# Kernel optimization log

Measured on AMD Instinct MI355X. Metric: run time of the kernel, lower is better.

The kernel has to match this reference:

```python
import jax, jax.numpy as jnp
import numpy as np

B, L, D = 4, 2048, 1024


def setup_inputs() -> dict:
    key = jax.random.key(0)
    ks = jax.random.split(key, 7)
    scale = 1.0 / np.sqrt(D)
    x = jax.random.normal(ks[0], (B, L, D), dtype=jnp.float32)
    wq = jax.random.normal(ks[1], (D, D), dtype=jnp.float32) * scale
    wk = jax.random.normal(ks[2], (D, D), dtype=jnp.float32) * scale
    wv = jax.random.normal(ks[3], (D, D), dtype=jnp.float32) * scale
    bq = jnp.zeros((D,), dtype=jnp.float32)
    bk = jnp.zeros((D,), dtype=jnp.float32)
    bv = jnp.zeros((D,), dtype=jnp.float32)
    # causal decoder mask, shape [B, 1, L, L] as produced by nn.make_causal_mask
    causal = jnp.tril(jnp.ones((L, L), dtype=bool))
    mask = jnp.broadcast_to(causal[None, None, :, :], (B, 1, L, L))
    return {"x": x, "mask": mask, "wq": wq, "bq": bq, "wk": wk, "bk": bk, "wv": wv, "bv": bv}


def reference(x, mask, wq, bq, wk, bk, wv, bv):
    # q/k/v projections (Dense with bias)
    q = x @ wq + bq            # [B, L, D]
    k = x @ wk + bk
    v = x @ wv + bv
    depth = q.shape[-1]
    q = q / jnp.sqrt(jnp.asarray(depth, dtype=q.dtype))
    attn = jnp.einsum('bqd,bkd->bqk', q, k)          # [B, L, L]
    attn = jnp.where(jnp.squeeze(mask), attn, -999999)
    attn = jax.nn.softmax(attn, axis=-1)
    out = attn @ v                                    # [B, L, D]
    return out
```

## Files before the change

kernel.cpp:

```cpp
#include <hip/hip_runtime.h>

typedef __bf16 bf16_t;
typedef __attribute__((ext_vector_type(8))) __bf16 bf16x8;
typedef __attribute__((ext_vector_type(4))) __bf16 bf16x4;
typedef __attribute__((ext_vector_type(4))) float f32x4;

#define B_  4
#define L_  2048
#define D_  1024
#define M_  (B_*L_)
#define N3_ (3*D_)

__device__ __forceinline__ void gload_lds16(const void* g, void* l) {
  __builtin_amdgcn_global_load_lds(
      (__attribute__((address_space(1))) void*)(g),
      (__attribute__((address_space(3))) void*)(l), 16, 0, 0);
}

__device__ __forceinline__ void stage_half(const bf16_t* __restrict__ g, int ld, int grow0,
                                           int k0, bf16_t* lds_tile, int h, int tid) {
  const int lane = tid & 63;
  const int csrc = ((lane & 7) ^ (lane >> 3)) << 3;
  const int rsub = tid >> 3;
  bf16_t* l0 = lds_tile + (size_t)(h * 128 + ((tid >> 6) << 3)) * 64;
  const bf16_t* g0 = g + (size_t)(grow0 + h * 128 + rsub) * ld + (k0 + csrc);
  gload_lds16(g0, l0);
  gload_lds16(g0 + (size_t)64 * ld, l0 + 64 * 64);
}

#define KTILE(J, AC, AN1, AN2, BCr, BNx, bC, bN)                                  \
  do {                                                                            \
    const int j_ = (J);                                                           \
    _Pragma("unroll")                                                             \
    for (int mi = 0; mi < 4; ++mi) {                                              \
      aM1_[mi][0] = *(const bf16x8*)(AC + abase + (4 + mi) * 2048 + co0);         \
      aM1_[mi][1] = *(const bf16x8*)(AC + abase + (4 + mi) * 2048 + co1);         \
    }                                                                             \
    if (j_ + 2 < NT) {                                                            \
      stage_half(A, lda, r0, (j_ + 2) * 64, AN2, 0, tid);                         \
      stage_half(A, lda, r0, (j_ + 2) * 64, AN2, 1, tid);                         \
    }                                                                             \
    asm volatile("s_waitcnt lgkmcnt(8)" ::: "memory");                            \
    __builtin_amdgcn_sched_barrier(0);                                            \
    __builtin_amdgcn_s_setprio(1);                                                \
    _Pragma("unroll")                                                             \
    for (int mi = 0; mi < 4; ++mi)                                                \
      _Pragma("unroll")                                                           \
      for (int ni = 0; ni < 2; ++ni) {                                            \
        acc[mi][ni] = __builtin_amdgcn_mfma_f32_16x16x32_bf16(                    \
            bC[ni][0], aM0_[mi][0], acc[mi][ni], 0, 0, 0);                        \
        acc[mi][ni] = __builtin_amdgcn_mfma_f32_16x16x32_bf16(                    \
            bC[ni][1], aM0_[mi][1], acc[mi][ni], 0, 0, 0);                        \
      }                                                                           \
    __builtin_amdgcn_s_setprio(0);                                                \
    if (j_ + 2 < NT) asm volatile("s_waitcnt vmcnt(4)" ::: "memory");             \
    else             asm volatile("s_waitcnt vmcnt(0)" ::: "memory");             \
    asm volatile("s_barrier" ::: "memory");                                       \
    if (j_ + 1 < NT) {                                                            \
      _Pragma("unroll")                                                           \
      for (int mi = 0; mi < 4; ++mi) {                                            \
        aM0_[mi][0] = *(const bf16x8*)(AN1 + abase + mi * 2048 + co0);            \
        aM0_[mi][1] = *(const bf16x8*)(AN1 + abase + mi * 2048 + co1);            \
      }                                                                           \
      _Pragma("unroll")                                                           \
      for (int ni = 0; ni < 2; ++ni) {                                            \
        bN[ni][0] = *(const bf16x8*)(BNx + bbase + ni * 1024 + co0);              \
        bN[ni][1] = *(const bf16x8*)(BNx + bbase + ni * 1024 + co1);              \
      }                                                                           \
      if (j_ + 2 < NT)                                                            \
        stage_half(Bt, ldb, c0, (j_ + 2) * 64, BCr, 0, tid);                      \
      asm volatile("s_waitcnt lgkmcnt(12)" ::: "memory");                         \
    } else {                                                                      \
      asm volatile("s_waitcnt lgkmcnt(0)" ::: "memory");                          \
    }                                                                             \
    __builtin_amdgcn_sched_barrier(0);                                            \
    __builtin_amdgcn_s_setprio(1);                                                \
    _Pragma("unroll")                                                             \
    for (int mi = 0; mi < 4; ++mi)                                                \
      _Pragma("unroll")                                                           \
      for (int ni = 0; ni < 2; ++ni) {                                            \
        acc[4 + mi][ni] = __builtin_amdgcn_mfma_f32_16x16x32_bf16(                \
            bC[ni][0], aM1_[mi][0], acc[4 + mi][ni], 0, 0, 0);                    \
        acc[4 + mi][ni] = __builtin_amdgcn_mfma_f32_16x16x32_bf16(                \
            bC[ni][1], aM1_[mi][1], acc[4 + mi][ni], 0, 0, 0);                    \
      }                                                                           \
    __builtin_amdgcn_s_setprio(0);                                                \
    asm volatile("s_barrier" ::: "memory");                                       \
  } while (0)

template<bool OUT_BF16, bool CAUSAL, bool VARK, bool PROJ>
__global__ __launch_bounds__(512, 2)
void gemm8(const bf16_t* __restrict__ A, int lda, long sA,
           const bf16_t* __restrict__ Bt, int ldb, long sB,
           void* __restrict__ Cv, int ldc, long sC,
           const float* __restrict__ b0, const float* __restrict__ b1,
           const float* __restrict__ b2, int K)
{
  const int gx = gridDim.x;
  const int nwg = gx * gridDim.y;
  const int orig = blockIdx.y * gx + blockIdx.x;
  const int swz = (orig & 7) * (nwg >> 3) + (orig >> 3);
  const int bx = swz % gx, by = swz / gx;
  if (CAUSAL && bx > 2 * by + 1) return;

  const int z = blockIdx.z;
  A  += (size_t)z * sA;
  Bt += (size_t)z * sB;

  const int r0 = by * 256, c0 = bx * 128;
  const int kend = VARK ? min(K, r0 + 256) : K;
  const int NT = kend >> 6;

  extern __shared__ __align__(16) bf16_t smem[];
  bf16_t* Ab0 = smem;
  bf16_t* Ab1 = smem + 16384;
  bf16_t* Ab2 = smem + 32768;
  bf16_t* Bb0 = smem + 49152;
  bf16_t* Bb1 = smem + 57344;

  const int tid = threadIdx.x;
  const int wid = tid >> 6, lane = tid & 63;
  const int wm = wid >> 2, wn = wid & 3;
  const int rl = lane & 15, cg = lane >> 4, x0 = lane & 7;
  const int co0 = ((cg ^ x0) << 3);
  const int co1 = (((4 + cg) ^ x0) << 3);
  const int abase = (wm * 16 + rl) * 64;
  const int bbase = (wn * 32 + rl) * 64;

  f32x4 acc[8][2] = {};
  bf16x8 aM0_[4][2], aM1_[4][2];
  bf16x8 bA_[2][2], bB_[2][2];

  stage_half(A,  lda, r0, 0,  Ab0, 0, tid);
  stage_half(A,  lda, r0, 0,  Ab0, 1, tid);
  stage_half(Bt, ldb, c0, 0,  Bb0, 0, tid);
  stage_half(A,  lda, r0, 64, Ab1, 0, tid);
  stage_half(A,  lda, r0, 64, Ab1, 1, tid);
  stage_half(Bt, ldb, c0, 64, Bb1, 0, tid);
  asm volatile("s_waitcnt vmcnt(6)" ::: "memory");
  asm volatile("s_barrier" ::: "memory");
  #pragma unroll
  for (int mi = 0; mi < 4; ++mi) {
    aM0_[mi][0] = *(const bf16x8*)(Ab0 + abase + mi * 2048 + co0);
    aM0_[mi][1] = *(const bf16x8*)(Ab0 + abase + mi * 2048 + co1);
  }
  #pragma unroll
  for (int ni = 0; ni < 2; ++ni) {
    bA_[ni][0] = *(const bf16x8*)(Bb0 + bbase + ni * 1024 + co0);
    bA_[ni][1] = *(const bf16x8*)(Bb0 + bbase + ni * 1024 + co1);
  }

  bf16_t *A0 = Ab0, *A1 = Ab1, *A2 = Ab2;
  for (int j = 0; j < NT; j += 2) {
    KTILE(j,     A0, A1, A2, Bb0, Bb1, bA_, bB_);
    KTILE(j + 1, A1, A2, A0, Bb1, Bb0, bB_, bA_);
    bf16_t* t = A2; A2 = A1; A1 = A0; A0 = t;
  }

  const int ml = lane & 15, ng = cg * 4;
  #pragma unroll
  for (int mi = 0; mi < 8; ++mi) {
    const int r = r0 + mi * 32 + wm * 16 + ml;
    #pragma unroll
    for (int ni = 0; ni < 2; ++ni) {
      const int c = c0 + wn * 32 + ni * 16 + ng;
      f32x4 v = acc[mi][ni];
      if (PROJ) {
        const float* bias = (c < D_) ? b0 : (c < 2 * D_) ? b1 : b2;
        const float4 bb = *(const float4*)(bias + (c & (D_ - 1)));
        const float sc = (c < D_) ? 0.03125f : 1.0f;
        v[0] = (v[0] + bb.x) * sc; v[1] = (v[1] + bb.y) * sc;
        v[2] = (v[2] + bb.z) * sc; v[3] = (v[3] + bb.w) * sc;
      }
      if (OUT_BF16) {
        bf16x4 o = {(bf16_t)v[0], (bf16_t)v[1], (bf16_t)v[2], (bf16_t)v[3]};
        *(bf16x4*)((bf16_t*)Cv + (size_t)z * sC + (size_t)r * ldc + c) = o;
      } else {
        *(f32x4*)((float*)Cv + (size_t)z * sC + (size_t)r * ldc + c) = v;
      }
    }
  }
}

__device__ __forceinline__ float blk_red_max(float v, float* red, int lane, int wid) {
  #pragma unroll
  for (int o = 32; o; o >>= 1) v = fmaxf(v, __shfl_down(v, o));
  __syncthreads();
  if (lane == 0) red[wid] = v;
  __syncthreads();
  return fmaxf(fmaxf(red[0], red[1]), fmaxf(red[2], red[3]));
}
__device__ __forceinline__ float blk_red_sum(float v, float* red, int lane, int wid) {
  #pragma unroll
  for (int o = 32; o; o >>= 1) v += __shfl_down(v, o);
  __syncthreads();
  if (lane == 0) red[wid] = v;
  __syncthreads();
  return red[0] + red[1] + red[2] + red[3];
}

__global__ __launch_bounds__(256)
void softmax_causal(const bf16_t* __restrict__ S, bf16_t* __restrict__ P) {
  const int r = blockIdx.x;
  const int n = r + 1;
  const int kend = min(((n + 255) >> 8) << 8, L_);
  const bf16_t* row = S + (size_t)blockIdx.y * L_ * L_ + (size_t)r * L_;
  bf16_t* prow = P + (size_t)blockIdx.y * L_ * L_ + (size_t)r * L_;
  const int tid = threadIdx.x, lane = tid & 63, wid = tid >> 6;
  __shared__ float red[4];

  float s[8];
  #pragma unroll
  for (int i = 0; i < 8; ++i) {
    const int c = tid + i * 256;
    s[i] = (c < n) ? (float)row[c] : -3.402823466e38f;
  }
  float mx = -3.402823466e38f;
  #pragma unroll
  for (int i = 0; i < 8; ++i) mx = fmaxf(mx, s[i]);
  mx = blk_red_max(mx, red, lane, wid);

  float e[8]; float sum = 0.f;
  #pragma unroll
  for (int i = 0; i < 8; ++i) {
    const int c = tid + i * 256;
    const float v = (c < n) ? __expf(s[i] - mx) : 0.f;
    e[i] = v; sum += v;
  }
  sum = blk_red_sum(sum, red, lane, wid);
  const float inv = 1.0f / sum;
  #pragma unroll
  for (int i = 0; i < 8; ++i) {
    const int c = tid + i * 256;
    if (c < kend) prow[c] = (bf16_t)(e[i] * inv);
  }
}

__global__ void cvt_f32_bf16(const float* __restrict__ in, bf16_t* __restrict__ out, int n4) {
  const int stride = gridDim.x * blockDim.x;
  for (int i = blockIdx.x * blockDim.x + threadIdx.x; i < n4; i += stride) {
    const float4 v = ((const float4*)in)[i];
    bf16x4 o = { (bf16_t)v.x, (bf16_t)v.y, (bf16_t)v.z, (bf16_t)v.w };
    ((bf16x4*)out)[i] = o;
  }
}

__global__ void transpose_w3(const float* __restrict__ w0, const float* __restrict__ w1,
                             const float* __restrict__ w2, bf16_t* __restrict__ oT) {
  const float* w = blockIdx.z == 0 ? w0 : (blockIdx.z == 1 ? w1 : w2);
  bf16_t* o = oT + (size_t)blockIdx.z * D_ * D_;
  __shared__ float t[32][33];
  const int tx = threadIdx.x, ty = threadIdx.y;
  const int x  = blockIdx.x * 32 + tx;
  const int y0 = blockIdx.y * 32;
  #pragma unroll
  for (int j = 0; j < 4; ++j)
    t[ty + j * 8][tx] = w[(size_t)(y0 + ty + j * 8) * D_ + x];
  __syncthreads();
  const int x2 = y0 + tx;
  const int y2 = blockIdx.x * 32;
  #pragma unroll
  for (int j = 0; j < 4; ++j)
    o[(size_t)(y2 + ty + j * 8) * D_ + x2] = (bf16_t)t[tx][ty + j * 8];
}

__global__ void transpose_bf16(const bf16_t* __restrict__ in, int ld_in, int coff,
                               bf16_t* __restrict__ out, int R, int C) {
  __shared__ bf16_t t[32][34];
  const int tx = threadIdx.x, ty = threadIdx.y;
  const int x  = blockIdx.x * 32 + tx;
  const int y0 = blockIdx.y * 32;
  #pragma unroll
  for (int j = 0; j < 4; ++j)
    t[ty + j * 8][tx] = in[(size_t)(y0 + ty + j * 8) * ld_in + coff + x];
  __syncthreads();
  const int x2 = y0 + tx;
  const int y2 = blockIdx.x * 32;
  #pragma unroll
  for (int j = 0; j < 4; ++j)
    out[(size_t)(y2 + ty + j * 8) * R + x2] = t[tx][ty + j * 8];
}

extern "C" void kernel_launch(void* const* d_in, const int* in_sizes, int n_in,
                              void* d_out, int out_size, void* d_ws, size_t ws_size,
                              hipStream_t stream) {
  const float* x  = (const float*)d_in[0];
  const float* wq = (const float*)d_in[2];
  const float* bq = (const float*)d_in[3];
  const float* wk = (const float*)d_in[4];
  const float* bk = (const float*)d_in[5];
  const float* wv = (const float*)d_in[6];
  const float* bv = (const float*)d_in[7];
  float* out = (float*)d_out;

  bf16_t* xb   = (bf16_t*)d_ws;
  bf16_t* wT   = xb  + (size_t)M_ * D_;
  bf16_t* qkv  = wT  + (size_t)N3_ * D_;
  bf16_t* vbT  = qkv + (size_t)M_ * N3_;
  bf16_t* Sb   = vbT + (size_t)M_ * D_;
  bf16_t* Pfull = qkv;

  const size_t SMEM = 131072;

  cvt_f32_bf16<<<1024, 256, 0, stream>>>(x, xb, M_ * D_ / 4);
  transpose_w3<<<dim3(32, 32, 3), dim3(32, 8), 0, stream>>>(wq, wk, wv, wT);

  gemm8<true, false, false, true><<<dim3(N3_ / 128, M_ / 256), 512, SMEM, stream>>>(
      xb, D_, 0, wT, D_, 0, qkv, N3_, 0, bq, bk, bv, D_);

  transpose_bf16<<<dim3(D_ / 32, M_ / 32), dim3(32, 8), 0, stream>>>(qkv, N3_, 2 * D_, vbT, M_, D_);

  gemm8<true, true, false, false><<<dim3(L_ / 128, L_ / 256, B_), 512, SMEM, stream>>>(
      qkv, N3_, (long)L_ * N3_, qkv + D_, N3_, (long)L_ * N3_, Sb, L_, (long)L_ * L_,
      nullptr, nullptr, nullptr, D_);

  softmax_causal<<<dim3(L_, B_), 256, 0, stream>>>(Sb, Pfull);

  gemm8<false, false, true, false><<<dim3(D_ / 128, L_ / 256, B_), 512, SMEM, stream>>>(
      Pfull, L_, (long)L_ * L_, vbT, M_, (long)L_, out, D_, (long)L_ * D_,
      nullptr, nullptr, nullptr, L_);
}
```

Measured before the change: 184.0 us.

## Split-K the PV GEMM with atomic accumulation and rebalance wave tiling to 64x64

The P·V GEMM is split into two K halves across doubled grid z, and each half adds its partial result into the fp32 output with atomicAdd. The output is zeroed with a memset beforehand. This is meant to spread the causally imbalanced, variable-K work across more workgroups. All GEMMs also change their wave arrangement from 4x2 waves of 128x32 to 2x4 waves of 64x64, which cuts LDS fragment loads per MFMA. The cost is atomic traffic, an extra memset, and a nondeterministic summation order.

```diff
diff --git a/kernel.cpp b/kernel.cpp
--- a/kernel.cpp
+++ b/kernel.cpp
@@ -32,25 +32,25 @@
   do {                                                                            \
     const int j_ = (J);                                                           \
     _Pragma("unroll")                                                             \
-    for (int mi = 0; mi < 4; ++mi) {                                              \
-      aM1_[mi][0] = *(const bf16x8*)(AC + abase + (4 + mi) * 2048 + co0);         \
-      aM1_[mi][1] = *(const bf16x8*)(AC + abase + (4 + mi) * 2048 + co1);         \
+    for (int mi = 0; mi < 2; ++mi) {                                              \
+      aHi_[mi][0] = *(const bf16x8*)(AC + abase + (2 + mi) * 1024 + co0);         \
+      aHi_[mi][1] = *(const bf16x8*)(AC + abase + (2 + mi) * 1024 + co1);         \
     }                                                                             \
     if (j_ + 2 < NT) {                                                            \
       stage_half(A, lda, r0, (j_ + 2) * 64, AN2, 0, tid);                         \
       stage_half(A, lda, r0, (j_ + 2) * 64, AN2, 1, tid);                         \
     }                                                                             \
-    asm volatile("s_waitcnt lgkmcnt(8)" ::: "memory");                            \
+    asm volatile("s_waitcnt lgkmcnt(4)" ::: "memory");                            \
     __builtin_amdgcn_sched_barrier(0);                                            \
     __builtin_amdgcn_s_setprio(1);                                                \
     _Pragma("unroll")                                                             \
-    for (int mi = 0; mi < 4; ++mi)                                                \
+    for (int mi = 0; mi < 2; ++mi)                                                \
       _Pragma("unroll")                                                           \
-      for (int ni = 0; ni < 2; ++ni) {                                            \
+      for (int ni = 0; ni < 4; ++ni) {                                            \
         acc[mi][ni] = __builtin_amdgcn_mfma_f32_16x16x32_bf16(                    \
-            bC[ni][0], aM0_[mi][0], acc[mi][ni], 0, 0, 0);                        \
+            bC[ni][0], aLo_[mi][0], acc[mi][ni], 0, 0, 0);                        \
         acc[mi][ni] = __builtin_amdgcn_mfma_f32_16x16x32_bf16(                    \
-            bC[ni][1], aM0_[mi][1], acc[mi][ni], 0, 0, 0);                        \
+            bC[ni][1], aLo_[mi][1], acc[mi][ni], 0, 0, 0);                        \
       }                                                                           \
     __builtin_amdgcn_s_setprio(0);                                                \
     if (j_ + 2 < NT) asm volatile("s_waitcnt vmcnt(4)" ::: "memory");             \
@@ -58,12 +58,12 @@
     asm volatile("s_barrier" ::: "memory");                                       \
     if (j_ + 1 < NT) {                                                            \
       _Pragma("unroll")                                                           \
-      for (int mi = 0; mi < 4; ++mi) {                                            \
-        aM0_[mi][0] = *(const bf16x8*)(AN1 + abase + mi * 2048 + co0);            \
-        aM0_[mi][1] = *(const bf16x8*)(AN1 + abase + mi * 2048 + co1);            \
+      for (int mi = 0; mi < 2; ++mi) {                                            \
+        aLo_[mi][0] = *(const bf16x8*)(AN1 + abase + mi * 1024 + co0);            \
+        aLo_[mi][1] = *(const bf16x8*)(AN1 + abase + mi * 1024 + co1);            \
       }                                                                           \
       _Pragma("unroll")                                                           \
-      for (int ni = 0; ni < 2; ++ni) {                                            \
+      for (int ni = 0; ni < 4; ++ni) {                                            \
         bN[ni][0] = *(const bf16x8*)(BNx + bbase + ni * 1024 + co0);              \
         bN[ni][1] = *(const bf16x8*)(BNx + bbase + ni * 1024 + co1);              \
       }                                                                           \
@@ -76,19 +76,19 @@
     __builtin_amdgcn_sched_barrier(0);                                            \
     __builtin_amdgcn_s_setprio(1);                                                \
     _Pragma("unroll")                                                             \
-    for (int mi = 0; mi < 4; ++mi)                                                \
+    for (int mi = 0; mi < 2; ++mi)                                                \
       _Pragma("unroll")                                                           \
-      for (int ni = 0; ni < 2; ++ni) {                                            \
-        acc[4 + mi][ni] = __builtin_amdgcn_mfma_f32_16x16x32_bf16(                \
-            bC[ni][0], aM1_[mi][0], acc[4 + mi][ni], 0, 0, 0);                    \
-        acc[4 + mi][ni] = __builtin_amdgcn_mfma_f32_16x16x32_bf16(                \
-            bC[ni][1], aM1_[mi][1], acc[4 + mi][ni], 0, 0, 0);                    \
+      for (int ni = 0; ni < 4; ++ni) {                                            \
+        acc[2 + mi][ni] = __builtin_amdgcn_mfma_f32_16x16x32_bf16(                \
+            bC[ni][0], aHi_[mi][0], acc[2 + mi][ni], 0, 0, 0);                    \
+        acc[2 + mi][ni] = __builtin_amdgcn_mfma_f32_16x16x32_bf16(                \
+            bC[ni][1], aHi_[mi][1], acc[2 + mi][ni], 0, 0, 0);                    \
       }                                                                           \
     __builtin_amdgcn_s_setprio(0);                                                \
     asm volatile("s_barrier" ::: "memory");                                       \
   } while (0)
 
-template<bool OUT_BF16, bool CAUSAL, bool VARK, bool PROJ>
+template<bool OUT_BF16, bool CAUSAL, bool VARK, bool PROJ, bool SPLITK>
 __global__ __launch_bounds__(512, 2)
 void gemm8(const bf16_t* __restrict__ A, int lda, long sA,
            const bf16_t* __restrict__ Bt, int ldb, long sB,
@@ -103,13 +103,16 @@
   const int bx = swz % gx, by = swz / gx;
   if (CAUSAL && bx > 2 * by + 1) return;
 
-  const int z = blockIdx.z;
+  int z = blockIdx.z, half = 0;
+  if (SPLITK) { half = z & 1; z >>= 1; }
   A  += (size_t)z * sA;
   Bt += (size_t)z * sB;
 
   const int r0 = by * 256, c0 = bx * 128;
   const int kend = VARK ? min(K, r0 + 256) : K;
-  const int NT = kend >> 6;
+  const int NTfull = kend >> 6;
+  int j0 = 0, NT = NTfull;
+  if (SPLITK) { const int mid = NTfull >> 1; j0 = half ? mid : 0; NT = half ? NTfull : mid; }
 
   extern __shared__ __align__(16) bf16_t smem[];
   bf16_t* Ab0 = smem;
@@ -120,38 +123,38 @@
 
   const int tid = threadIdx.x;
   const int wid = tid >> 6, lane = tid & 63;
-  const int wm = wid >> 2, wn = wid & 3;
+  const int wm = wid >> 1, wn = wid & 1;
   const int rl = lane & 15, cg = lane >> 4, x0 = lane & 7;
   const int co0 = ((cg ^ x0) << 3);
   const int co1 = (((4 + cg) ^ x0) << 3);
-  const int abase = (wm * 16 + rl) * 64;
-  const int bbase = (wn * 32 + rl) * 64;
-
-  f32x4 acc[8][2] = {};
-  bf16x8 aM0_[4][2], aM1_[4][2];
-  bf16x8 bA_[2][2], bB_[2][2];
-
-  stage_half(A,  lda, r0, 0,  Ab0, 0, tid);
-  stage_half(A,  lda, r0, 0,  Ab0, 1, tid);
-  stage_half(Bt, ldb, c0, 0,  Bb0, 0, tid);
-  stage_half(A,  lda, r0, 64, Ab1, 0, tid);
-  stage_half(A,  lda, r0, 64, Ab1, 1, tid);
-  stage_half(Bt, ldb, c0, 64, Bb1, 0, tid);
+  const int abase = (wm * 64 + rl) * 64;
+  const int bbase = (wn * 64 + rl) * 64;
+
+  f32x4 acc[4][4] = {};
+  bf16x8 aLo_[2][2], aHi_[2][2];
+  bf16x8 bA_[4][2], bB_[4][2];
+
+  stage_half(A,  lda, r0, j0 * 64,       Ab0, 0, tid);
+  stage_half(A,  lda, r0, j0 * 64,       Ab0, 1, tid);
+  stage_half(Bt, ldb, c0, j0 * 64,       Bb0, 0, tid);
+  stage_half(A,  lda, r0, (j0 + 1) * 64, Ab1, 0, tid);
+  stage_half(A,  lda, r0, (j0 + 1) * 64, Ab1, 1, tid);
+  stage_half(Bt, ldb, c0, (j0 + 1) * 64, Bb1, 0, tid);
   asm volatile("s_waitcnt vmcnt(6)" ::: "memory");
   asm volatile("s_barrier" ::: "memory");
   #pragma unroll
-  for (int mi = 0; mi < 4; ++mi) {
-    aM0_[mi][0] = *(const bf16x8*)(Ab0 + abase + mi * 2048 + co0);
-    aM0_[mi][1] = *(const bf16x8*)(Ab0 + abase + mi * 2048 + co1);
-  }
-  #pragma unroll
-  for (int ni = 0; ni < 2; ++ni) {
+  for (int mi = 0; mi < 2; ++mi) {
+    aLo_[mi][0] = *(const bf16x8*)(Ab0 + abase + mi * 1024 + co0);
+    aLo_[mi][1] = *(const bf16x8*)(Ab0 + abase + mi * 1024 + co1);
+  }
+  #pragma unroll
+  for (int ni = 0; ni < 4; ++ni) {
     bA_[ni][0] = *(const bf16x8*)(Bb0 + bbase + ni * 1024 + co0);
     bA_[ni][1] = *(const bf16x8*)(Bb0 + bbase + ni * 1024 + co1);
   }
 
   bf16_t *A0 = Ab0, *A1 = Ab1, *A2 = Ab2;
-  for (int j = 0; j < NT; j += 2) {
+  for (int j = j0; j < NT; j += 2) {
     KTILE(j,     A0, A1, A2, Bb0, Bb1, bA_, bB_);
     KTILE(j + 1, A1, A2, A0, Bb1, Bb0, bB_, bA_);
     bf16_t* t = A2; A2 = A1; A1 = A0; A0 = t;
@@ -159,11 +162,11 @@
 
   const int ml = lane & 15, ng = cg * 4;
   #pragma unroll
-  for (int mi = 0; mi < 8; ++mi) {
-    const int r = r0 + mi * 32 + wm * 16 + ml;
+  for (int mi = 0; mi < 4; ++mi) {
+    const int r = r0 + wm * 64 + mi * 16 + ml;
     #pragma unroll
-    for (int ni = 0; ni < 2; ++ni) {
-      const int c = c0 + wn * 32 + ni * 16 + ng;
+    for (int ni = 0; ni < 4; ++ni) {
+      const int c = c0 + wn * 64 + ni * 16 + ng;
       f32x4 v = acc[mi][ni];
       if (PROJ) {
         const float* bias = (c < D_) ? b0 : (c < 2 * D_) ? b1 : b2;
@@ -172,7 +175,11 @@
         v[0] = (v[0] + bb.x) * sc; v[1] = (v[1] + bb.y) * sc;
         v[2] = (v[2] + bb.z) * sc; v[3] = (v[3] + bb.w) * sc;
       }
-      if (OUT_BF16) {
+      if (SPLITK) {
+        float* p = (float*)Cv + (size_t)z * sC + (size_t)r * ldc + c;
+        atomicAdd(p + 0, v[0]); atomicAdd(p + 1, v[1]);
+        atomicAdd(p + 2, v[2]); atomicAdd(p + 3, v[3]);
+      } else if (OUT_BF16) {
         bf16x4 o = {(bf16_t)v[0], (bf16_t)v[1], (bf16_t)v[2], (bf16_t)v[3]};
         *(bf16x4*)((bf16_t*)Cv + (size_t)z * sC + (size_t)r * ldc + c) = o;
       } else {
@@ -302,21 +309,23 @@
 
   const size_t SMEM = 131072;
 
+  hipMemsetAsync(d_out, 0, (size_t)out_size * sizeof(float), stream);
+
   cvt_f32_bf16<<<1024, 256, 0, stream>>>(x, xb, M_ * D_ / 4);
   transpose_w3<<<dim3(32, 32, 3), dim3(32, 8), 0, stream>>>(wq, wk, wv, wT);
 
-  gemm8<true, false, false, true><<<dim3(N3_ / 128, M_ / 256), 512, SMEM, stream>>>(
+  gemm8<true, false, false, true, false><<<dim3(N3_ / 128, M_ / 256), 512, SMEM, stream>>>(
       xb, D_, 0, wT, D_, 0, qkv, N3_, 0, bq, bk, bv, D_);
 
   transpose_bf16<<<dim3(D_ / 32, M_ / 32), dim3(32, 8), 0, stream>>>(qkv, N3_, 2 * D_, vbT, M_, D_);
 
-  gemm8<true, true, false, false><<<dim3(L_ / 128, L_ / 256, B_), 512, SMEM, stream>>>(
+  gemm8<true, true, false, false, false><<<dim3(L_ / 128, L_ / 256, B_), 512, SMEM, stream>>>(
       qkv, N3_, (long)L_ * N3_, qkv + D_, N3_, (long)L_ * N3_, Sb, L_, (long)L_ * L_,
       nullptr, nullptr, nullptr, D_);
 
   softmax_causal<<<dim3(L_, B_), 256, 0, stream>>>(Sb, Pfull);
 
-  gemm8<false, false, true, false><<<dim3(D_ / 128, L_ / 256, B_), 512, SMEM, stream>>>(
+  gemm8<false, false, true, false, true><<<dim3(D_ / 128, L_ / 256, B_ * 2), 512, SMEM, stream>>>(
       Pfull, L_, (long)L_ * L_, vbT, M_, (long)L_, out, D_, (long)L_ * D_,
       nullptr, nullptr, nullptr, L_);
 }
```

After: 372.0 us. 2.02x slower.

## Add 256x256-tile GEMM kernel for the fused QKV projection

Applied to the files above, without the earlier changes.

Adds a dedicated gemm256 kernel with 256x256 output tiles for the QKV projection. It triple-buffers A and double-buffers B in LDS and splits each k-step into two MFMA halves, overlapping fragment loads with the next stage. Larger tiles raise arithmetic intensity and cut redundant global/LDS traffic per output element versus the previous 256x128 tiles. In exchange it uses 160KB of LDS, which with launch bounds of 2 per CU may limit occupancy, and the grid shrinks to 12x32 workgroups, which may underfill the GPU. The bias/scale epilogue moves from the generic gemm8 template into the new kernel.

```diff
diff --git a/kernel.cpp b/kernel.cpp
--- a/kernel.cpp
+++ b/kernel.cpp
@@ -26,6 +26,135 @@
   const bf16_t* g0 = g + (size_t)(grow0 + h * 128 + rsub) * ld + (k0 + csrc);
   gload_lds16(g0, l0);
   gload_lds16(g0 + (size_t)64 * ld, l0 + 64 * 64);
+}
+
+__global__ __launch_bounds__(512, 2)
+void gemm256(const bf16_t* __restrict__ A, int lda,
+             const bf16_t* __restrict__ Bt, int ldb,
+             bf16_t* __restrict__ C, int ldc,
+             const float* __restrict__ b0, const float* __restrict__ b1,
+             const float* __restrict__ b2, int K)
+{
+  const int gx = gridDim.x;
+  const int nwg = gx * gridDim.y;
+  const int orig = blockIdx.y * gx + blockIdx.x;
+  const int swz = (orig & 7) * (nwg >> 3) + (orig >> 3);
+  const int bx = swz % gx, by = swz / gx;
+
+  const int r0 = by * 256, c0 = bx * 256;
+  const int NT = K >> 6;
+
+  extern __shared__ __align__(16) bf16_t smem[];
+  bf16_t* A0 = smem;
+  bf16_t* A1 = smem + 16384;
+  bf16_t* A2 = smem + 32768;
+  bf16_t* B0 = smem + 49152;
+  bf16_t* B1 = smem + 65536;
+
+  const int tid = threadIdx.x;
+  const int wid = tid >> 6, lane = tid & 63;
+  const int wm = wid >> 2, wn = wid & 3;
+  const int rl = lane & 15, cg = lane >> 4, x0 = lane & 7;
+  const int co0 = ((cg ^ x0) << 3);
+  const int co1 = (((4 + cg) ^ x0) << 3);
+  const int aoff = (wm * 128 + rl) * 64;
+  const int boff = (wn * 64 + rl) * 64;
+
+  f32x4 acc[8][4] = {};
+  bf16x8 aLo_[4][2], aHi_[4][2], bF[4][2];
+
+  stage_half(A,  lda, r0, 0,  A0, 0, tid);  stage_half(A,  lda, r0, 0,  A0, 1, tid);
+  stage_half(Bt, ldb, c0, 0,  B0, 0, tid);  stage_half(Bt, ldb, c0, 0,  B0, 1, tid);
+  stage_half(A,  lda, r0, 64, A1, 0, tid);  stage_half(A,  lda, r0, 64, A1, 1, tid);
+  stage_half(Bt, ldb, c0, 64, B1, 0, tid);  stage_half(Bt, ldb, c0, 64, B1, 1, tid);
+  asm volatile("s_waitcnt vmcnt(8)" ::: "memory");
+  asm volatile("s_barrier" ::: "memory");
+  #pragma unroll
+  for (int mi = 0; mi < 4; ++mi) {
+    aLo_[mi][0] = *(const bf16x8*)(A0 + aoff + mi * 1024 + co0);
+    aLo_[mi][1] = *(const bf16x8*)(A0 + aoff + mi * 1024 + co1);
+  }
+
+  for (int j = 0; j < NT; ++j) {
+    #pragma unroll
+    for (int ni = 0; ni < 4; ++ni) {
+      bF[ni][0] = *(const bf16x8*)(B0 + boff + ni * 1024 + co0);
+      bF[ni][1] = *(const bf16x8*)(B0 + boff + ni * 1024 + co1);
+    }
+    #pragma unroll
+    for (int mi = 0; mi < 4; ++mi) {
+      aHi_[mi][0] = *(const bf16x8*)(A0 + aoff + (4 + mi) * 1024 + co0);
+      aHi_[mi][1] = *(const bf16x8*)(A0 + aoff + (4 + mi) * 1024 + co1);
+    }
+    if (j + 2 < NT) {
+      stage_half(A, lda, r0, (j + 2) * 64, A2, 0, tid);
+      stage_half(A, lda, r0, (j + 2) * 64, A2, 1, tid);
+    }
+    asm volatile("s_waitcnt lgkmcnt(0)" ::: "memory");
+    __builtin_amdgcn_sched_barrier(0);
+    __builtin_amdgcn_s_setprio(1);
+    #pragma unroll
+    for (int mi = 0; mi < 4; ++mi)
+      #pragma unroll
+      for (int ni = 0; ni < 4; ++ni) {
+        acc[mi][ni] = __builtin_amdgcn_mfma_f32_16x16x32_bf16(
+            bF[ni][0], aLo_[mi][0], acc[mi][ni], 0, 0, 0);
+        acc[mi][ni] = __builtin_amdgcn_mfma_f32_16x16x32_bf16(
+            bF[ni][1], aLo_[mi][1], acc[mi][ni], 0, 0, 0);
+      }
+    __builtin_amdgcn_s_setprio(0);
+    if (j + 2 < NT) asm volatile("s_waitcnt vmcnt(4)" ::: "memory");
+    else            asm volatile("s_waitcnt vmcnt(0)" ::: "memory");
+    asm volatile("s_barrier" ::: "memory");
+
+    if (j + 1 < NT) {
+      #pragma unroll
+      for (int mi = 0; mi < 4; ++mi) {
+        aLo_[mi][0] = *(const bf16x8*)(A1 + aoff + mi * 1024 + co0);
+        aLo_[mi][1] = *(const bf16x8*)(A1 + aoff + mi * 1024 + co1);
+      }
+      if (j + 2 < NT) {
+        stage_half(Bt, ldb, c0, (j + 2) * 64, B0, 0, tid);
+        stage_half(Bt, ldb, c0, (j + 2) * 64, B0, 1, tid);
+      }
+      asm volatile("s_waitcnt lgkmcnt(8)" ::: "memory");
+    } else {
+      asm volatile("s_waitcnt lgkmcnt(0)" ::: "memory");
+    }
+    __builtin_amdgcn_sched_barrier(0);
+    __builtin_amdgcn_s_setprio(1);
+    #pragma unroll
+    for (int mi = 0; mi < 4; ++mi)
+      #pragma unroll
+      for (int ni = 0; ni < 4; ++ni) {
+        acc[4 + mi][ni] = __builtin_amdgcn_mfma_f32_16x16x32_bf16(
+            bF[ni][0], aHi_[mi][0], acc[4 + mi][ni], 0, 0, 0);
+        acc[4 + mi][ni] = __builtin_amdgcn_mfma_f32_16x16x32_bf16(
+            bF[ni][1], aHi_[mi][1], acc[4 + mi][ni], 0, 0, 0);
+      }
+    __builtin_amdgcn_s_setprio(0);
+    asm volatile("s_barrier" ::: "memory");
+
+    bf16_t* t = A0; A0 = A1; A1 = A2; A2 = t;
+    t = B0; B0 = B1; B1 = t;
+  }
+
+  const int ng = cg * 4;
+  #pragma unroll
+  for (int mi = 0; mi < 8; ++mi) {
+    const int r = r0 + wm * 128 + mi * 16 + rl;
+    #pragma unroll
+    for (int ni = 0; ni < 4; ++ni) {
+      const int c = c0 + wn * 64 + ni * 16 + ng;
+      const float* bias = (c < D_) ? b0 : (c < 2 * D_) ? b1 : b2;
+      const float4 bb = *(const float4*)(bias + (c & (D_ - 1)));
+      const float sc = (c < D_) ? 0.03125f : 1.0f;
+      f32x4 v = acc[mi][ni];
+      bf16x4 o = {(bf16_t)((v[0] + bb.x) * sc), (bf16_t)((v[1] + bb.y) * sc),
+                  (bf16_t)((v[2] + bb.z) * sc), (bf16_t)((v[3] + bb.w) * sc)};
+      *(bf16x4*)(C + (size_t)r * ldc + c) = o;
+    }
+  }
 }
 
 #define KTILE(J, AC, AN1, AN2, BCr, BNx, bC, bN)                                  \
@@ -88,13 +217,11 @@
     asm volatile("s_barrier" ::: "memory");                                       \
   } while (0)
 
-template<bool OUT_BF16, bool CAUSAL, bool VARK, bool PROJ>
+template<bool OUT_BF16, bool CAUSAL, bool VARK>
 __global__ __launch_bounds__(512, 2)
 void gemm8(const bf16_t* __restrict__ A, int lda, long sA,
            const bf16_t* __restrict__ Bt, int ldb, long sB,
-           void* __restrict__ Cv, int ldc, long sC,
-           const float* __restrict__ b0, const float* __restrict__ b1,
-           const float* __restrict__ b2, int K)
+           void* __restrict__ Cv, int ldc, long sC, int K)
 {
   const int gx = gridDim.x;
   const int nwg = gx * gridDim.y;
@@ -165,13 +292,6 @@
     for (int ni = 0; ni < 2; ++ni) {
       const int c = c0 + wn * 32 + ni * 16 + ng;
       f32x4 v = acc[mi][ni];
-      if (PROJ) {
-        const float* bias = (c < D_) ? b0 : (c < 2 * D_) ? b1 : b2;
-        const float4 bb = *(const float4*)(bias + (c & (D_ - 1)));
-        const float sc = (c < D_) ? 0.03125f : 1.0f;
-        v[0] = (v[0] + bb.x) * sc; v[1] = (v[1] + bb.y) * sc;
-        v[2] = (v[2] + bb.z) * sc; v[3] = (v[3] + bb.w) * sc;
-      }
       if (OUT_BF16) {
         bf16x4 o = {(bf16_t)v[0], (bf16_t)v[1], (bf16_t)v[2], (bf16_t)v[3]};
         *(bf16x4*)((bf16_t*)Cv + (size_t)z * sC + (size_t)r * ldc + c) = o;
@@ -300,23 +420,33 @@
   bf16_t* Sb   = vbT + (size_t)M_ * D_;
   bf16_t* Pfull = qkv;
 
-  const size_t SMEM = 131072;
+  const size_t SMEM128 = 131072;
+  const size_t SMEM256 = 163840;
+
+  static bool attr_done = false;
+  if (!attr_done) {
+    hipFuncSetAttribute((const void*)gemm256,
+                        hipFuncAttributeMaxDynamicSharedMemorySize, (int)SMEM256);
+    hipFuncSetAttribute((const void*)gemm8<true, true, false>,
+                        hipFuncAttributeMaxDynamicSharedMemorySize, (int)SMEM128);
+    hipFuncSetAttribute((const void*)gemm8<false, false, true>,
+                        hipFuncAttributeMaxDynamicSharedMemorySize, (int)SMEM128);
+    attr_done = true;
+  }
 
   cvt_f32_bf16<<<1024, 256, 0, stream>>>(x, xb, M_ * D_ / 4);
   transpose_w3<<<dim3(32, 32, 3), dim3(32, 8), 0, stream>>>(wq, wk, wv, wT);
 
-  gemm8<true, false, false, true><<<dim3(N3_ / 128, M_ / 256), 512, SMEM, stream>>>(
-      xb, D_, 0, wT, D_, 0, qkv, N3_, 0, bq, bk, bv, D_);
+  gemm256<<<dim3(N3_ / 256, M_ / 256), 512, SMEM256, stream>>>(
+      xb, D_, wT, D_, qkv, N3_, bq, bk, bv, D_);
 
   transpose_bf16<<<dim3(D_ / 32, M_ / 32), dim3(32, 8), 0, stream>>>(qkv, N3_, 2 * D_, vbT, M_, D_);
 
-  gemm8<true, true, false, false><<<dim3(L_ / 128, L_ / 256, B_), 512, SMEM, stream>>>(
-      qkv, N3_, (long)L_ * N3_, qkv + D_, N3_, (long)L_ * N3_, Sb, L_, (long)L_ * L_,
-      nullptr, nullptr, nullptr, D_);
+  gemm8<true, true, false><<<dim3(L_ / 128, L_ / 256, B_), 512, SMEM128, stream>>>(
+      qkv, N3_, (long)L_ * N3_, qkv + D_, N3_, (long)L_ * N3_, Sb, L_, (long)L_ * L_, D_);
 
   softmax_causal<<<dim3(L_, B_), 256, 0, stream>>>(Sb, Pfull);
 
-  gemm8<false, false, true, false><<<dim3(D_ / 128, L_ / 256, B_), 512, SMEM, stream>>>(
-      Pfull, L_, (long)L_ * L_, vbT, M_, (long)L_, out, D_, (long)L_ * D_,
-      nullptr, nullptr, nullptr, L_);
-}
+  gemm8<false, false, true><<<dim3(D_ / 128, L_ / 256, B_), 512, SMEM128, stream>>>(
+      Pfull, L_, (long)L_ * L_, vbT, M_, (long)L_, out, D_, (long)L_ * D_, L_);
+}
```

Result: slower. 189.2 us (+2.8%).

## Split-K the causal PV GEMM for long rows and vectorize softmax loads

Applied to the files above, without the earlier changes.

The PV GEMM grid grows from 8 to 12 row blocks. The four longest causal row blocks have their K range split in half: the second half is written to an fp32 partial buffer that reuses the S region, and a new add_partial kernel folds it into the output. This balances the triangular workload across workgroups, at the cost of an extra launch and an extra fp32 read-modify-write of half the output. Softmax now loads and stores 8 contiguous bf16 values per thread as one vector instead of strided scalar accesses.

```diff
diff --git a/kernel.cpp b/kernel.cpp
--- a/kernel.cpp
+++ b/kernel.cpp
@@ -88,11 +88,12 @@
     asm volatile("s_barrier" ::: "memory");                                       \
   } while (0)
 
-template<bool OUT_BF16, bool CAUSAL, bool VARK, bool PROJ>
+template<bool OUT_BF16, bool CAUSAL, bool VARK, bool PROJ, bool PVS>
 __global__ __launch_bounds__(512, 2)
 void gemm8(const bf16_t* __restrict__ A, int lda, long sA,
            const bf16_t* __restrict__ Bt, int ldb, long sB,
            void* __restrict__ Cv, int ldc, long sC,
+           float* __restrict__ part,
            const float* __restrict__ b0, const float* __restrict__ b1,
            const float* __restrict__ b2, int K)
 {
@@ -100,7 +101,17 @@
   const int nwg = gx * gridDim.y;
   const int orig = blockIdx.y * gx + blockIdx.x;
   const int swz = (orig & 7) * (nwg >> 3) + (orig >> 3);
-  const int bx = swz % gx, by = swz / gx;
+  const int bx = swz % gx, yy = swz / gx;
+
+  int by, j0, NT;
+  if (PVS) {
+    if (yy < 8) { by = yy; const int NTf = 4 * (by + 1); j0 = 0; NT = (by >= 4) ? (NTf >> 1) : NTf; }
+    else        { by = yy - 4; const int NTf = 4 * (by + 1); j0 = NTf >> 1; NT = NTf; }
+  } else {
+    by = yy; j0 = 0;
+    const int kend = VARK ? min(K, by * 256 + 256) : K;
+    NT = kend >> 6;
+  }
   if (CAUSAL && bx > 2 * by + 1) return;
 
   const int z = blockIdx.z;
@@ -108,8 +119,6 @@
   Bt += (size_t)z * sB;
 
   const int r0 = by * 256, c0 = bx * 128;
-  const int kend = VARK ? min(K, r0 + 256) : K;
-  const int NT = kend >> 6;
 
   extern __shared__ __align__(16) bf16_t smem[];
   bf16_t* Ab0 = smem;
@@ -131,12 +140,12 @@
   bf16x8 aM0_[4][2], aM1_[4][2];
   bf16x8 bA_[2][2], bB_[2][2];
 
-  stage_half(A,  lda, r0, 0,  Ab0, 0, tid);
-  stage_half(A,  lda, r0, 0,  Ab0, 1, tid);
-  stage_half(Bt, ldb, c0, 0,  Bb0, 0, tid);
-  stage_half(A,  lda, r0, 64, Ab1, 0, tid);
-  stage_half(A,  lda, r0, 64, Ab1, 1, tid);
-  stage_half(Bt, ldb, c0, 64, Bb1, 0, tid);
+  stage_half(A,  lda, r0, j0 * 64,       Ab0, 0, tid);
+  stage_half(A,  lda, r0, j0 * 64,       Ab0, 1, tid);
+  stage_half(Bt, ldb, c0, j0 * 64,       Bb0, 0, tid);
+  stage_half(A,  lda, r0, (j0 + 1) * 64, Ab1, 0, tid);
+  stage_half(A,  lda, r0, (j0 + 1) * 64, Ab1, 1, tid);
+  stage_half(Bt, ldb, c0, (j0 + 1) * 64, Bb1, 0, tid);
   asm volatile("s_waitcnt vmcnt(6)" ::: "memory");
   asm volatile("s_barrier" ::: "memory");
   #pragma unroll
@@ -151,7 +160,7 @@
   }
 
   bf16_t *A0 = Ab0, *A1 = Ab1, *A2 = Ab2;
-  for (int j = 0; j < NT; j += 2) {
+  for (int j = j0; j < NT; j += 2) {
     KTILE(j,     A0, A1, A2, Bb0, Bb1, bA_, bB_);
     KTILE(j + 1, A1, A2, A0, Bb1, Bb0, bB_, bA_);
     bf16_t* t = A2; A2 = A1; A1 = A0; A0 = t;
@@ -172,7 +181,12 @@
         v[0] = (v[0] + bb.x) * sc; v[1] = (v[1] + bb.y) * sc;
         v[2] = (v[2] + bb.z) * sc; v[3] = (v[3] + bb.w) * sc;
       }
-      if (OUT_BF16) {
+      if (PVS) {
+        float* dst = (yy < 8)
+            ? (float*)Cv + (size_t)z * sC + (size_t)r * ldc + c
+            : part + (size_t)z * (1024 * 1024) + (size_t)(r - 1024) * 1024 + c;
+        *(f32x4*)dst = v;
+      } else if (OUT_BF16) {
         bf16x4 o = {(bf16_t)v[0], (bf16_t)v[1], (bf16_t)v[2], (bf16_t)v[3]};
         *(bf16x4*)((bf16_t*)Cv + (size_t)z * sC + (size_t)r * ldc + c) = o;
       } else {
@@ -180,6 +194,17 @@
       }
     }
   }
+}
+
+__global__ void add_partial(float* __restrict__ out, const float* __restrict__ part) {
+  const int i = blockIdx.x * blockDim.x + threadIdx.x;
+  const int z = i >> 18;
+  const int o = i & 262143;
+  float4* dst = (float4*)(out + (size_t)z * L_ * D_ + 1024 * D_) + o;
+  const float4 p = ((const float4*)(part + (size_t)z * 1024 * 1024))[o];
+  float4 d = *dst;
+  d.x += p.x; d.y += p.y; d.z += p.z; d.w += p.w;
+  *dst = d;
 }
 
 __device__ __forceinline__ float blk_red_max(float v, float* red, int lane, int wid) {
@@ -207,32 +232,34 @@
   const bf16_t* row = S + (size_t)blockIdx.y * L_ * L_ + (size_t)r * L_;
   bf16_t* prow = P + (size_t)blockIdx.y * L_ * L_ + (size_t)r * L_;
   const int tid = threadIdx.x, lane = tid & 63, wid = tid >> 6;
+  const int c0 = tid * 8;
   __shared__ float red[4];
 
+  const bf16x8 v8 = *(const bf16x8*)(row + c0);
   float s[8];
   #pragma unroll
+  for (int i = 0; i < 8; ++i)
+    s[i] = (c0 + i < n) ? (float)v8[i] : -3.402823466e38f;
+
+  float mx = s[0];
+  #pragma unroll
+  for (int i = 1; i < 8; ++i) mx = fmaxf(mx, s[i]);
+  mx = blk_red_max(mx, red, lane, wid);
+
+  float e[8]; float sum = 0.f;
+  #pragma unroll
   for (int i = 0; i < 8; ++i) {
-    const int c = tid + i * 256;
-    s[i] = (c < n) ? (float)row[c] : -3.402823466e38f;
-  }
-  float mx = -3.402823466e38f;
-  #pragma unroll
-  for (int i = 0; i < 8; ++i) mx = fmaxf(mx, s[i]);
-  mx = blk_red_max(mx, red, lane, wid);
-
-  float e[8]; float sum = 0.f;
-  #pragma unroll
-  for (int i = 0; i < 8; ++i) {
-    const int c = tid + i * 256;
-    const float v = (c < n) ? __expf(s[i] - mx) : 0.f;
+    const float v = (c0 + i < n) ? __expf(s[i] - mx) : 0.f;
     e[i] = v; sum += v;
   }
   sum = blk_red_sum(sum, red, lane, wid);
   const float inv = 1.0f / sum;
-  #pragma unroll
-  for (int i = 0; i < 8; ++i) {
-    const int c = tid + i * 256;
-    if (c < kend) prow[c] = (bf16_t)(e[i] * inv);
+
+  if (c0 < kend) {
+    bf16x8 o;
+    #pragma unroll
+    for (int i = 0; i < 8; ++i) o[i] = (bf16_t)(e[i] * inv);
+    *(bf16x8*)(prow + c0) = o;
   }
 }
 
@@ -299,24 +326,27 @@
   bf16_t* vbT  = qkv + (size_t)M_ * N3_;
   bf16_t* Sb   = vbT + (size_t)M_ * D_;
   bf16_t* Pfull = qkv;
+  float*  part = (float*)Sb;
 
   const size_t SMEM = 131072;
 
   cvt_f32_bf16<<<1024, 256, 0, stream>>>(x, xb, M_ * D_ / 4);
   transpose_w3<<<dim3(32, 32, 3), dim3(32, 8), 0, stream>>>(wq, wk, wv, wT);
 
-  gemm8<true, false, false, true><<<dim3(N3_ / 128, M_ / 256), 512, SMEM, stream>>>(
-      xb, D_, 0, wT, D_, 0, qkv, N3_, 0, bq, bk, bv, D_);
+  gemm8<true, false, false, true, false><<<dim3(N3_ / 128, M_ / 256), 512, SMEM, stream>>>(
+      xb, D_, 0, wT, D_, 0, qkv, N3_, 0, nullptr, bq, bk, bv, D_);
 
   transpose_bf16<<<dim3(D_ / 32, M_ / 32), dim3(32, 8), 0, stream>>>(qkv, N3_, 2 * D_, vbT, M_, D_);
 
-  gemm8<true, true, false, false><<<dim3(L_ / 128, L_ / 256, B_), 512, SMEM, stream>>>(
+  gemm8<true, true, false, false, false><<<dim3(L_ / 128, L_ / 256, B_), 512, SMEM, stream>>>(
       qkv, N3_, (long)L_ * N3_, qkv + D_, N3_, (long)L_ * N3_, Sb, L_, (long)L_ * L_,
-      nullptr, nullptr, nullptr, D_);
+      nullptr, nullptr, nullptr, nullptr, D_);
 
   softmax_causal<<<dim3(L_, B_), 256, 0, stream>>>(Sb, Pfull);
 
-  gemm8<false, false, true, false><<<dim3(D_ / 128, L_ / 256, B_), 512, SMEM, stream>>>(
+  gemm8<false, false, false, false, true><<<dim3(D_ / 128, 12, B_), 512, SMEM, stream>>>(
       Pfull, L_, (long)L_ * L_, vbT, M_, (long)L_, out, D_, (long)L_ * D_,
-      nullptr, nullptr, nullptr, L_);
-}
+      part, nullptr, nullptr, nullptr, L_);
+
+  add_partial<<<4096, 256, 0, stream>>>(out, part);
+}
```

Result: slower. 189.1 us (+2.8%).
